# Kernel tuning notes

Hardware: AMD Instinct MI355X
Metric: run time of the kernel (lower is better)

The kernel has to match this reference:

```python
import jax, jax.numpy as jnp
import numpy as np

N = 100000
E = 1600000
IN_C = 256
OUT_C = 128


def setup_inputs() -> dict:
    key = jax.random.key(0)
    k1, k2, k3 = jax.random.split(key, 3)
    x = jax.random.normal(k1, (N, IN_C), dtype=jnp.float32)
    edge_index = jax.random.randint(k2, (2, E), 0, N, dtype=jnp.int64)
    # Linear(in_channels, out_channels, bias=False): weight is [out, in]
    bound = 1.0 / np.sqrt(IN_C)
    weight = jax.random.uniform(k3, (OUT_C, IN_C), dtype=jnp.float32,
                                minval=-bound, maxval=bound)
    return {"x": x, "edge_index": edge_index, "weight": weight}


def reference(x, edge_index, weight):
    # Feature transform: x @ W.T  -> [N, OUT_C]
    h = x @ weight.T

    row, col = edge_index[0], edge_index[1]  # source, target

    # GCN normalization (add_self_loops=False, edge_weight=None -> ones)
    ones_e = jnp.ones((E,), dtype=h.dtype)
    deg = jax.ops.segment_sum(ones_e, col, num_segments=N)  # in-degree
    deg_inv_sqrt = jnp.where(deg > 0, jax.lax.rsqrt(deg), 0.0)
    ew = deg_inv_sqrt[row] * deg_inv_sqrt[col]  # [E]

    # Message passing: gather-multiply-scatter-add
    msgs = h[row] * ew[:, None]                       # [E, OUT_C]
    out = jax.ops.segment_sum(msgs, col, num_segments=N)  # [N, OUT_C]

    # Complex-to-real trick: negate second half, roll by half
    half = OUT_C // 2
    multiplier = jnp.concatenate([jnp.ones((half,), h.dtype),
                                  -jnp.ones((half,), h.dtype)])
    out = out * multiplier[None, :]
    out = jnp.roll(out, half, axis=-1)
    return out
```

## Files before the change

kernel.cpp:

```cpp
#include <hip/hip_runtime.h>
#include <hip/hip_bf16.h>

#define NN 100000
#define EE 1600000
#define INC 256
#define OUTC 128
#define NBUK 782
#define NPB  256
#define CHUNK ((EE + NPB - 1) / NPB)

typedef short bf16x8 __attribute__((ext_vector_type(8)));
typedef float f32x4 __attribute__((ext_vector_type(4)));

static __device__ __forceinline__ unsigned short f2bf(float f){
    unsigned u = __builtin_bit_cast(unsigned, f);
    u += 0x7fffu + ((u >> 16) & 1u);
    return (unsigned short)(u >> 16);
}
static __device__ __forceinline__ float bf2f(unsigned short h){
    unsigned u = ((unsigned)h) << 16;
    return __builtin_bit_cast(float, u);
}

__global__ void hist_kernel(const int* __restrict__ col, unsigned* __restrict__ bcnt){
    __shared__ unsigned h[NBUK];
    for (int i = threadIdx.x; i < NBUK; i += 256) h[i] = 0;
    __syncthreads();
    for (int i = blockIdx.x*blockDim.x + threadIdx.x; i < EE; i += gridDim.x*blockDim.x)
        atomicAdd(&h[((unsigned)col[i]) >> 7], 1u);
    __syncthreads();
    for (int i = threadIdx.x; i < NBUK; i += 256)
        if (h[i]) atomicAdd(&bcnt[i], h[i]);
}

__global__ void scanb_kernel(const unsigned* __restrict__ bcnt,
                             unsigned* __restrict__ base, unsigned* __restrict__ cursor){
    __shared__ unsigned tmp[1024];
    int t = threadIdx.x;
    unsigned v = (t < NBUK) ? bcnt[t] : 0u;
    tmp[t] = v;
    __syncthreads();
    for (int off = 1; off < 1024; off <<= 1){
        unsigned x = (t >= off) ? tmp[t-off] : 0u;
        __syncthreads();
        tmp[t] += x;
        __syncthreads();
    }
    if (t < NBUK){ unsigned ex = tmp[t] - v; base[t] = ex; cursor[t] = ex; }
    if (t == 0) base[NBUK] = EE;
}

__global__ void partition_kernel(const int* __restrict__ ei, unsigned* __restrict__ cursor,
                                 unsigned* __restrict__ packed){
    __shared__ unsigned cnt[NBUK], gpos[NBUK], cnt2[NBUK];
    int t = threadIdx.x;
    int s = blockIdx.x*CHUNK, e = min(s + CHUNK, EE);
    for (int i = t; i < NBUK; i += 256){ cnt[i] = 0; cnt2[i] = 0; }
    __syncthreads();
    for (int i = s + t; i < e; i += 256)
        atomicAdd(&cnt[((unsigned)ei[EE + i]) >> 7], 1u);
    __syncthreads();
    for (int i = t; i < NBUK; i += 256){
        unsigned c = cnt[i];
        gpos[i] = c ? atomicAdd(&cursor[i], c) : 0u;
    }
    __syncthreads();
    for (int i = s + t; i < e; i += 256){
        unsigned c = (unsigned)ei[EE + i];
        unsigned r = (unsigned)ei[i];
        unsigned b = c >> 7;
        unsigned rk = atomicAdd(&cnt2[b], 1u);
        packed[gpos[b] + rk] = ((c & 127u) << 24) | r;
    }
}

__global__ void sort_kernel(const unsigned* __restrict__ packed, const unsigned* __restrict__ base,
                            unsigned* __restrict__ erow, unsigned* __restrict__ noffs,
                            float* __restrict__ dinv){
    __shared__ unsigned cnt[128], cur[128], tmp[128];
    int t = threadIdx.x;
    unsigned s = base[blockIdx.x], e = base[blockIdx.x + 1];
    if (t < 128) cnt[t] = 0;
    __syncthreads();
    for (unsigned i = s + t; i < e; i += 256)
        atomicAdd(&cnt[packed[i] >> 24], 1u);
    __syncthreads();
    if (t < 128) tmp[t] = cnt[t];
    __syncthreads();
    for (int off = 1; off < 128; off <<= 1){
        unsigned v = (t >= off && t < 128) ? tmp[t-off] : 0u;
        __syncthreads();
        if (t < 128) tmp[t] += v;
        __syncthreads();
    }
    if (t < 128){
        unsigned ex = s + tmp[t] - cnt[t];
        cur[t] = ex;
        int node = blockIdx.x*128 + t;
        if (node < NN){
            noffs[node] = ex;
            dinv[node] = cnt[t] ? rsqrtf((float)cnt[t]) : 0.f;
        }
    }
    if (blockIdx.x == 0 && t == 0) noffs[NN] = EE;
    __syncthreads();
    for (unsigned i = s + t; i < e; i += 256){
        unsigned u = packed[i];
        unsigned pos = atomicAdd(&cur[u >> 24], 1u);
        erow[pos] = u & 0xFFFFFFu;
    }
}

__global__ void wprep_kernel(const float* __restrict__ w, unsigned short* __restrict__ wfrag){
    int idx = blockIdx.x*256 + threadIdx.x;
    if (idx < 8*8*64*8){
        int r = idx & 7, l = (idx >> 3) & 63, t = (idx >> 9) & 7, s = idx >> 12;
        int n = t*16 + (l & 15);
        int k = s*32 + ((l >> 4) << 3) + r;
        wfrag[idx] = f2bf(w[n*INC + k]);
    }
}

__launch_bounds__(256)
__global__ void gemm_kernel(const float* __restrict__ x, const unsigned short* __restrict__ wfrag,
                            const float* __restrict__ dinv,
                            unsigned short* __restrict__ h2, int Nn){
    __shared__ float xs[2][4096];
    int tid = threadIdx.x;
    int wv = tid >> 6, lane = tid & 63;
    int row0 = blockIdx.x*64;
    int rrow = wv*16 + (lane & 15);
    int kg2 = lane >> 4;
    const bf16x8* wf = (const bf16x8*)wfrag;

    f32x4 acc[8];
    #pragma unroll
    for (int t = 0; t < 8; ++t) acc[t] = (f32x4){0.f,0.f,0.f,0.f};

    auto stage = [&](int sl, int buf){
        #pragma unroll
        for (int j = 0; j < 4; ++j){
            int L = (wv*4 + j)*64 + lane;
            int srow = L >> 4;
            int cslot = L & 15;
            int kchunk = cslot ^ (srow & 15);
            const float* g = x + (size_t)min(row0 + srow, Nn-1)*INC + sl*64 + kchunk*4;
            __builtin_amdgcn_global_load_lds(g, &xs[buf][(wv*4 + j)*256], 16, 0, 0);
        }
    };

    stage(0, 0);
    __syncthreads();

    for (int sl = 0; sl < 4; ++sl){
        int cur = sl & 1;
        if (sl < 3) stage(sl + 1, cur ^ 1);

        #pragma unroll
        for (int sg = 0; sg < 2; ++sg){
            int c0 = sg*8 + kg2*2;
            f32x4 a0 = *(const f32x4*)&xs[cur][rrow*64 + ((c0    ) ^ (rrow & 15))*4];
            f32x4 a1 = *(const f32x4*)&xs[cur][rrow*64 + ((c0 + 1) ^ (rrow & 15))*4];
            bf16x8 af;
            af[0]=f2bf(a0[0]); af[1]=f2bf(a0[1]); af[2]=f2bf(a0[2]); af[3]=f2bf(a0[3]);
            af[4]=f2bf(a1[0]); af[5]=f2bf(a1[1]); af[6]=f2bf(a1[2]); af[7]=f2bf(a1[3]);
            int s = sl*2 + sg;
            #pragma unroll
            for (int t = 0; t < 8; ++t){
                bf16x8 bf = wf[(s*8 + t)*64 + lane];
                acc[t] = __builtin_amdgcn_mfma_f32_16x16x32_bf16(af, bf, acc[t], 0, 0, 0);
            }
        }
        __syncthreads();
    }

    int rbase = row0 + wv*16 + ((lane >> 4) << 2);
    float sc[4];
    #pragma unroll
    for (int r = 0; r < 4; ++r){
        int row = rbase + r;
        sc[r] = (row < Nn) ? dinv[row] : 0.f;
    }
    #pragma unroll
    for (int t = 0; t < 8; ++t){
        int o  = t*16 + (lane & 15);
        int dc = (o + 64) & 127;
        float sgn = (o < 64) ? 1.f : -1.f;
        #pragma unroll
        for (int r = 0; r < 4; ++r){
            int row = rbase + r;
            if (row < Nn) h2[(size_t)row*OUTC + dc] = f2bf(sgn * sc[r] * acc[t][r]);
        }
    }
}

__launch_bounds__(256)
__global__ void gather_kernel(const unsigned short* __restrict__ h2,
                              const unsigned* __restrict__ noffs,
                              const unsigned* __restrict__ erow,
                              const float* __restrict__ dinv,
                              float* __restrict__ out, int Nn){
    int node = blockIdx.x*4 + (threadIdx.x >> 6);
    if (node >= Nn) return;
    int lane = threadIdx.x & 63;
    unsigned s = noffs[node], e = noffs[node+1];
    unsigned deg = e - s;
    const unsigned* h2u = (const unsigned*)h2;

    float lA0=0,lA1=0,lA2=0,lA3=0,lA4=0,lA5=0,lA6=0,lA7=0;
    float hA0=0,hA1=0,hA2=0,hA3=0,hA4=0,hA5=0,hA6=0,hA7=0;

    for (unsigned b = 0; b < deg; b += 64){
        unsigned my = b + lane;
        unsigned eidx = (my < deg) ? erow[s + my] : 0u;
        unsigned chunk = min(64u, deg - b);
        unsigned j = 0;
        for (; j + 8 <= chunk; j += 8){
            unsigned r0 = __shfl(eidx, (int)(j+0));
            unsigned r1 = __shfl(eidx, (int)(j+1));
            unsigned r2 = __shfl(eidx, (int)(j+2));
            unsigned r3 = __shfl(eidx, (int)(j+3));
            unsigned r4 = __shfl(eidx, (int)(j+4));
            unsigned r5 = __shfl(eidx, (int)(j+5));
            unsigned r6 = __shfl(eidx, (int)(j+6));
            unsigned r7 = __shfl(eidx, (int)(j+7));
            unsigned v0 = h2u[(size_t)r0*64 + lane];
            unsigned v1 = h2u[(size_t)r1*64 + lane];
            unsigned v2 = h2u[(size_t)r2*64 + lane];
            unsigned v3 = h2u[(size_t)r3*64 + lane];
            unsigned v4 = h2u[(size_t)r4*64 + lane];
            unsigned v5 = h2u[(size_t)r5*64 + lane];
            unsigned v6 = h2u[(size_t)r6*64 + lane];
            unsigned v7 = h2u[(size_t)r7*64 + lane];
            lA0 += bf2f((unsigned short)(v0 & 0xFFFFu)); hA0 += bf2f((unsigned short)(v0 >> 16));
            lA1 += bf2f((unsigned short)(v1 & 0xFFFFu)); hA1 += bf2f((unsigned short)(v1 >> 16));
            lA2 += bf2f((unsigned short)(v2 & 0xFFFFu)); hA2 += bf2f((unsigned short)(v2 >> 16));
            lA3 += bf2f((unsigned short)(v3 & 0xFFFFu)); hA3 += bf2f((unsigned short)(v3 >> 16));
            lA4 += bf2f((unsigned short)(v4 & 0xFFFFu)); hA4 += bf2f((unsigned short)(v4 >> 16));
            lA5 += bf2f((unsigned short)(v5 & 0xFFFFu)); hA5 += bf2f((unsigned short)(v5 >> 16));
            lA6 += bf2f((unsigned short)(v6 & 0xFFFFu)); hA6 += bf2f((unsigned short)(v6 >> 16));
            lA7 += bf2f((unsigned short)(v7 & 0xFFFFu)); hA7 += bf2f((unsigned short)(v7 >> 16));
        }
        for (; j < chunk; ++j){
            unsigned r = __shfl(eidx, (int)j);
            unsigned v = h2u[(size_t)r*64 + lane];
            lA0 += bf2f((unsigned short)(v & 0xFFFFu));
            hA0 += bf2f((unsigned short)(v >> 16));
        }
    }
    float lo = ((lA0+lA1)+(lA2+lA3)) + ((lA4+lA5)+(lA6+lA7));
    float hi = ((hA0+hA1)+(hA2+hA3)) + ((hA4+hA5)+(hA6+hA7));
    float wc = dinv[node];
    float2 o = {lo*wc, hi*wc};
    *(float2*)(out + (size_t)node*OUTC + lane*2) = o;
}

extern "C" void kernel_launch(void* const* d_in, const int* in_sizes, int n_in,
                              void* d_out, int out_size, void* d_ws, size_t ws_size,
                              hipStream_t stream){
    const float* x  = (const float*)d_in[0];
    const int*   ei = (const int*)d_in[1];
    const float* w  = (const float*)d_in[2];
    float* out = (float*)d_out;

    char* ws = (char*)d_ws;
    size_t off = 0;
    auto alloc = [&](size_t b) -> char* {
        char* p = ws + off;
        off += (b + 255) & ~(size_t)255;
        return p;
    };
    unsigned* bcnt   = (unsigned*)alloc((size_t)NBUK*4);
    unsigned* base   = (unsigned*)alloc((size_t)(NBUK+1)*4);
    unsigned* cursor = (unsigned*)alloc((size_t)NBUK*4);
    float*    dinv   = (float*)  alloc((size_t)NN*4);
    unsigned* packed = (unsigned*)alloc((size_t)EE*4);
    unsigned* erow   = (unsigned*)alloc((size_t)EE*4);
    unsigned* noffs  = (unsigned*)alloc((size_t)(NN+1)*4);
    unsigned short* wfrag = (unsigned short*)alloc((size_t)8*8*64*8*2);
    unsigned short* h2 = (unsigned short*)alloc((size_t)NN*OUTC*2);

    hipMemsetAsync(bcnt, 0, (size_t)NBUK*4, stream);
    wprep_kernel<<<128, 256, 0, stream>>>(w, wfrag);
    hist_kernel<<<256, 256, 0, stream>>>(ei + EE, bcnt);
    scanb_kernel<<<1, 1024, 0, stream>>>(bcnt, base, cursor);
    partition_kernel<<<NPB, 256, 0, stream>>>(ei, cursor, packed);
    sort_kernel<<<NBUK, 256, 0, stream>>>(packed, base, erow, noffs, dinv);
    gemm_kernel<<<(NN+63)/64, 256, 0, stream>>>(x, wfrag, dinv, h2, NN);
    gather_kernel<<<(NN+3)/4, 256, 0, stream>>>(h2, noffs, erow, dinv, out, NN);
}
```

Before: 162.4 us.

## Slice h2 into 16-column panels and gather per slice for cache locality

The GEMM now writes h2 as eight column slices, each a contiguous [N,16] bf16 panel, instead of row-major [N,128]. The gather kernel launches eight times as many blocks, and block index selects the slice. Each wave reads eight neighbors at once with 32-byte row segments and reduces across lane groups with shuffles. Each slice's working set (about 3.2 MB) is meant to fit better in L2 and cache during random gathers. In exchange, edge indices are re-read eight times and each access is a short 32-byte segment.

```diff
diff --git a/kernel.cpp b/kernel.cpp
--- a/kernel.cpp
+++ b/kernel.cpp
@@ -21,6 +21,12 @@
     unsigned u = ((unsigned)h) << 16;
     return __builtin_bit_cast(float, u);
 }
+static __device__ __forceinline__ float blo(unsigned u){
+    return __builtin_bit_cast(float, u << 16);
+}
+static __device__ __forceinline__ float bhi(unsigned u){
+    return __builtin_bit_cast(float, u & 0xFFFF0000u);
+}
 
 __global__ void hist_kernel(const int* __restrict__ col, unsigned* __restrict__ bcnt){
     __shared__ unsigned h[NBUK];
@@ -124,7 +130,7 @@
 __launch_bounds__(256)
 __global__ void gemm_kernel(const float* __restrict__ x, const unsigned short* __restrict__ wfrag,
                             const float* __restrict__ dinv,
-                            unsigned short* __restrict__ h2, int Nn){
+                            unsigned short* __restrict__ h2s, int Nn){
     __shared__ float xs[2][4096];
     int tid = threadIdx.x;
     int wv = tid >> 6, lane = tid & 63;
@@ -186,73 +192,66 @@
         int o  = t*16 + (lane & 15);
         int dc = (o + 64) & 127;
         float sgn = (o < 64) ? 1.f : -1.f;
+        int slice = dc >> 4, cis = dc & 15;
         #pragma unroll
         for (int r = 0; r < 4; ++r){
             int row = rbase + r;
-            if (row < Nn) h2[(size_t)row*OUTC + dc] = f2bf(sgn * sc[r] * acc[t][r]);
+            if (row < Nn)
+                h2s[((size_t)slice*NN + row)*16 + cis] = f2bf(sgn * sc[r] * acc[t][r]);
         }
     }
 }
 
 __launch_bounds__(256)
-__global__ void gather_kernel(const unsigned short* __restrict__ h2,
+__global__ void gather_kernel(const unsigned* __restrict__ h2su,
                               const unsigned* __restrict__ noffs,
                               const unsigned* __restrict__ erow,
                               const float* __restrict__ dinv,
-                              float* __restrict__ out, int Nn){
-    int node = blockIdx.x*4 + (threadIdx.x >> 6);
-    if (node >= Nn) return;
-    int lane = threadIdx.x & 63;
-    unsigned s = noffs[node], e = noffs[node+1];
-    unsigned deg = e - s;
-    const unsigned* h2u = (const unsigned*)h2;
-
-    float lA0=0,lA1=0,lA2=0,lA3=0,lA4=0,lA5=0,lA6=0,lA7=0;
-    float hA0=0,hA1=0,hA2=0,hA3=0,hA4=0,hA5=0,hA6=0,hA7=0;
-
-    for (unsigned b = 0; b < deg; b += 64){
-        unsigned my = b + lane;
-        unsigned eidx = (my < deg) ? erow[s + my] : 0u;
-        unsigned chunk = min(64u, deg - b);
-        unsigned j = 0;
-        for (; j + 8 <= chunk; j += 8){
-            unsigned r0 = __shfl(eidx, (int)(j+0));
-            unsigned r1 = __shfl(eidx, (int)(j+1));
-            unsigned r2 = __shfl(eidx, (int)(j+2));
-            unsigned r3 = __shfl(eidx, (int)(j+3));
-            unsigned r4 = __shfl(eidx, (int)(j+4));
-            unsigned r5 = __shfl(eidx, (int)(j+5));
-            unsigned r6 = __shfl(eidx, (int)(j+6));
-            unsigned r7 = __shfl(eidx, (int)(j+7));
-            unsigned v0 = h2u[(size_t)r0*64 + lane];
-            unsigned v1 = h2u[(size_t)r1*64 + lane];
-            unsigned v2 = h2u[(size_t)r2*64 + lane];
-            unsigned v3 = h2u[(size_t)r3*64 + lane];
-            unsigned v4 = h2u[(size_t)r4*64 + lane];
-            unsigned v5 = h2u[(size_t)r5*64 + lane];
-            unsigned v6 = h2u[(size_t)r6*64 + lane];
-            unsigned v7 = h2u[(size_t)r7*64 + lane];
-            lA0 += bf2f((unsigned short)(v0 & 0xFFFFu)); hA0 += bf2f((unsigned short)(v0 >> 16));
-            lA1 += bf2f((unsigned short)(v1 & 0xFFFFu)); hA1 += bf2f((unsigned short)(v1 >> 16));
-            lA2 += bf2f((unsigned short)(v2 & 0xFFFFu)); hA2 += bf2f((unsigned short)(v2 >> 16));
-            lA3 += bf2f((unsigned short)(v3 & 0xFFFFu)); hA3 += bf2f((unsigned short)(v3 >> 16));
-            lA4 += bf2f((unsigned short)(v4 & 0xFFFFu)); hA4 += bf2f((unsigned short)(v4 >> 16));
-            lA5 += bf2f((unsigned short)(v5 & 0xFFFFu)); hA5 += bf2f((unsigned short)(v5 >> 16));
-            lA6 += bf2f((unsigned short)(v6 & 0xFFFFu)); hA6 += bf2f((unsigned short)(v6 >> 16));
-            lA7 += bf2f((unsigned short)(v7 & 0xFFFFu)); hA7 += bf2f((unsigned short)(v7 >> 16));
-        }
-        for (; j < chunk; ++j){
-            unsigned r = __shfl(eidx, (int)j);
-            unsigned v = h2u[(size_t)r*64 + lane];
-            lA0 += bf2f((unsigned short)(v & 0xFFFFu));
-            hA0 += bf2f((unsigned short)(v >> 16));
-        }
-    }
-    float lo = ((lA0+lA1)+(lA2+lA3)) + ((lA4+lA5)+(lA6+lA7));
-    float hi = ((hA0+hA1)+(hA2+hA3)) + ((hA4+hA5)+(hA6+hA7));
-    float wc = dinv[node];
-    float2 o = {lo*wc, hi*wc};
-    *(float2*)(out + (size_t)node*OUTC + lane*2) = o;
+                              float* __restrict__ out){
+    int slice = blockIdx.x & 7;
+    int nb = blockIdx.x >> 3;
+    int wave = threadIdx.x >> 6, lane = threadIdx.x & 63;
+    int g8 = lane >> 3;
+    int cp = lane & 7;
+    const unsigned* hs = h2su + (size_t)slice*NN*8;
+
+    int node = nb*4 + wave;
+    if (node >= NN) return;
+    unsigned s = noffs[node];
+    unsigned deg = noffs[node+1] - s;
+
+    float aL=0.f, aH=0.f, bL=0.f, bH=0.f;
+    unsigned j = 0;
+    for (; j + 16 <= deg; j += 16){
+        unsigned ra = __builtin_nontemporal_load(erow + s + j + g8);
+        unsigned rb = __builtin_nontemporal_load(erow + s + j + 8 + g8);
+        unsigned va = hs[(size_t)ra*8 + cp];
+        unsigned vb = hs[(size_t)rb*8 + cp];
+        aL += blo(va); aH += bhi(va);
+        bL += blo(vb); bH += bhi(vb);
+    }
+    if (j + 8 <= deg){
+        unsigned ra = __builtin_nontemporal_load(erow + s + j + g8);
+        unsigned va = hs[(size_t)ra*8 + cp];
+        aL += blo(va); aH += bhi(va);
+        j += 8;
+    }
+    for (; j < deg; ++j){
+        unsigned r = erow[s + j];
+        unsigned v = hs[(size_t)r*8 + cp];
+        aL += (g8 == 0) ? blo(v) : 0.f;
+        aH += (g8 == 0) ? bhi(v) : 0.f;
+    }
+    aL += bL; aH += bH;
+    aL += __shfl_down(aL, 32); aH += __shfl_down(aH, 32);
+    aL += __shfl_down(aL, 16); aH += __shfl_down(aH, 16);
+    aL += __shfl_down(aL, 8);  aH += __shfl_down(aH, 8);
+    if (lane < 8){
+        float wc = dinv[node];
+        float* dst = out + (size_t)node*OUTC + slice*16 + cp*2;
+        __builtin_nontemporal_store(aL*wc, dst);
+        __builtin_nontemporal_store(aH*wc, dst + 1);
+    }
 }
 
 extern "C" void kernel_launch(void* const* d_in, const int* in_sizes, int n_in,
@@ -278,7 +277,7 @@
     unsigned* erow   = (unsigned*)alloc((size_t)EE*4);
     unsigned* noffs  = (unsigned*)alloc((size_t)(NN+1)*4);
     unsigned short* wfrag = (unsigned short*)alloc((size_t)8*8*64*8*2);
-    unsigned short* h2 = (unsigned short*)alloc((size_t)NN*OUTC*2);
+    unsigned short* h2s = (unsigned short*)alloc((size_t)NN*OUTC*2);
 
     hipMemsetAsync(bcnt, 0, (size_t)NBUK*4, stream);
     wprep_kernel<<<128, 256, 0, stream>>>(w, wfrag);
@@ -286,6 +285,6 @@
     scanb_kernel<<<1, 1024, 0, stream>>>(bcnt, base, cursor);
     partition_kernel<<<NPB, 256, 0, stream>>>(ei, cursor, packed);
     sort_kernel<<<NBUK, 256, 0, stream>>>(packed, base, erow, noffs, dinv);
-    gemm_kernel<<<(NN+63)/64, 256, 0, stream>>>(x, wfrag, dinv, h2, NN);
-    gather_kernel<<<(NN+3)/4, 256, 0, stream>>>(h2, noffs, erow, dinv, out, NN);
-}
+    gemm_kernel<<<(NN+63)/64, 256, 0, stream>>>(x, wfrag, dinv, h2s, NN);
+    gather_kernel<<<((NN+3)/4)*8, 256, 0, stream>>>((const unsigned*)h2s, noffs, erow, dinv, out);
+}
```

New measurement: 479.1 us. 195% more time.
